# Optimization experiments

Measured on AMD Instinct MI355X. Metric: run time of the kernel, lower is better.

The kernel has to match this reference:

```python
import jax, jax.numpy as jnp
import numpy as np

B, C, H, W = 2, 32, 256, 1216
PT = 6
EPS = 1e-6

def _conv(x, w):
    # 3x3 conv, stride 1, SAME padding, NCHW/OIHW
    return jax.lax.conv_general_dilated(x, w, (1, 1), ((1, 1), (1, 1)),
                                        dimension_numbers=('NCHW', 'OIHW', 'NCHW'))

def _cbn(x, w, s, b):
    # conv (bias=False) + eval-mode BatchNorm folded into per-channel scale/bias
    return _conv(x, w) * s[None, :, None, None] + b[None, :, None, None]

def _cb(x, w, b):
    # conv with bias (no norm branch of Basic2d)
    return _conv(x, w) + b[None, :, None, None]

def _gen_kernel(fout, w1, s1, b1, w2, s2, b2):
    # GenKernel: normalized per-pixel kernel with middle weight = 1 - sum(others)
    h = jax.nn.relu(_cbn(fout, w1, s1, b1))
    w = _cbn(h, w2, s2, b2)  # [B, pk*pk-1, H, W]
    w = w / (jnp.sum(jnp.abs(w), axis=1, keepdims=True) + EPS)
    wmid = 1.0 - jnp.sum(w, axis=1, keepdims=True)
    half = w.shape[1] // 2
    return jnp.concatenate([w[:, :half], wmid, w[:, half:]], axis=1)  # [B, pk*pk, H, W]

def _local_conv(x, w, k):
    # bpconvlocal: per-pixel spatially-varying k x k convolution of a 1-channel map
    p = k // 2
    _, _, Hx, Wx = x.shape
    xp = jnp.pad(x, ((0, 0), (0, 0), (p, p), (p, p)))
    patches = jnp.stack([xp[:, 0, i:i + Hx, j:j + Wx]
                         for i in range(k) for j in range(k)], axis=1)  # [B, k*k, H, W]
    return jnp.sum(w * patches, axis=1, keepdims=True)

def _cspn(fout, hn, h0,
          k3w1, k3s1, k3b1, k3w2, k3s2, k3b2,
          k5w1, k5s1, k5b1, k5w2, k5s2, k5b2,
          k7w1, k7s1, k7b1, k7w2, k7s2, k7b2,
          mw1, ms1, mb1, mw2, mbias2,
          cw1, cs1, cb1, cw2, cbias2,
          tw1, ts1, tb1, tw2, tbias2):
    w3 = _gen_kernel(fout, k3w1, k3s1, k3b1, k3w2, k3s2, k3b2)
    w5 = _gen_kernel(fout, k5w1, k5s1, k5b1, k5w2, k5s2, k5b2)
    w7 = _gen_kernel(fout, k7w1, k7s1, k7b1, k7w2, k7s2, k7b2)
    valid = (h0 > 0.001).astype(fout.dtype)
    mask = jax.nn.sigmoid(_cb(jax.nn.relu(_cbn(fout, mw1, ms1, mb1)), mw2, mbias2)) * valid
    m3, m5, m7 = jnp.split(mask, 3, axis=1)
    conf = jax.nn.softmax(_cb(jax.nn.relu(_cbn(fout, cw1, cs1, cb1)), cw2, cbias2), axis=1)
    c3, c5, c7 = jnp.split(conf, 3, axis=1)
    h3 = h5 = h7 = hn
    hns = [hn]
    for i in range(PT):
        h3 = (1.0 - m3) * _local_conv(h3, w3, 3) + m3 * h0
        h5 = (1.0 - m5) * _local_conv(h5, w5, 5) + m5 * h0
        h7 = (1.0 - m7) * _local_conv(h7, w7, 7) + m7 * h0
        if i == PT // 2 - 1:
            hns.append(c3 * h3 + c5 * h5 + c7 * h7)
    hns.append(c3 * h3 + c5 * h5 + c7 * h7)
    hns = jnp.concatenate(hns, axis=1)  # [B, 3, H, W]
    wt = jax.nn.softmax(_cb(jax.nn.relu(_cbn(jnp.concatenate([fout, hns], axis=1),
                                             tw1, ts1, tb1)), tw2, tbias2), axis=1)
    return jnp.sum(wt * hns, axis=1, keepdims=True)

def setup_inputs():
    key = jax.random.key(0)
    ks = iter(jax.random.split(key, 80))
    def nrm(shape, s=0.05):
        return jax.random.normal(next(ks), shape, dtype=jnp.float32) * s
    d = {}
    d['fout'] = jax.random.normal(next(ks), (B, C, H, W), dtype=jnp.float32)
    d['hn'] = jax.random.uniform(next(ks), (B, 1, H, W), dtype=jnp.float32) * 10.0
    sparse = (jax.random.uniform(next(ks), (B, 1, H, W)) < 0.06).astype(jnp.float32)
    d['h0'] = sparse * jax.random.uniform(next(ks), (B, 1, H, W), dtype=jnp.float32) * 10.0
    for pk, pre in ((3, 'k3'), (5, 'k5'), (7, 'k7')):
        co = pk * pk - 1
        d[pre + 'w1'] = nrm((C, C, 3, 3)); d[pre + 's1'] = 1.0 + nrm((C,)); d[pre + 'b1'] = nrm((C,))
        d[pre + 'w2'] = nrm((co, C, 3, 3)); d[pre + 's2'] = 1.0 + nrm((co,)); d[pre + 'b2'] = nrm((co,))
    for pre, cin in (('m', C), ('c', C), ('t', C + 3)):
        d[pre + 'w1'] = nrm((C, cin, 3, 3)); d[pre + 's1'] = 1.0 + nrm((C,)); d[pre + 'b1'] = nrm((C,))
        d[pre + 'w2'] = nrm((3, C, 3, 3)); d[pre + 'bias2'] = nrm((3,))
    return d

def reference(fout, hn, h0,
              k3w1, k3s1, k3b1, k3w2, k3s2, k3b2,
              k5w1, k5s1, k5b1, k5w2, k5s2, k5b2,
              k7w1, k7s1, k7b1, k7w2, k7s2, k7b2,
              mw1, ms1, mb1, mw2, mbias2,
              cw1, cs1, cb1, cw2, cbias2,
              tw1, ts1, tb1, tw2, tbias2):
    return _cspn(fout, hn, h0,
                 k3w1, k3s1, k3b1, k3w2, k3s2, k3b2,
                 k5w1, k5s1, k5b1, k5w2, k5s2, k5b2,
                 k7w1, k7s1, k7b1, k7w2, k7s2, k7b2,
                 mw1, ms1, mb1, mw2, mbias2,
                 cw1, cs1, cb1, cw2, cbias2,
                 tw1, ts1, tb1, tw2, tbias2)
```

## Files before the change

### kernel.cpp

```cpp
#include <hip/hip_runtime.h>
#include <hip/hip_bf16.h>

constexpr int B_ = 2, H_ = 256, W_ = 1216;
constexpr int HW = H_ * W_;
constexpr int NP = B_ * HW;
constexpr int WP = W_ + 2;
constexpr int HP = H_ + 2;
constexpr int HWP = HP * WP;
constexpr float EPS_ = 1e-6f;

constexpr int PW1_K3 = 0;
constexpr int PW1_K5 = 18432;
constexpr int PW1_K7 = 36864;
constexpr int PW2_K3 = 55296;
constexpr int PW2_K5 = 64512;
constexpr int PW2_K7 = 82944;
constexpr int PP1_M  = 110592;
constexpr int PP1_C  = 119808;
constexpr int PP1_T  = 129024;
constexpr int PP1T2  = 138240;
constexpr int PG2_M  = 140544;
constexpr int PG2_C  = 145152;
constexpr int PG2_T  = 149760;
constexpr int PREP_N = 154368;

typedef __bf16 bfrag __attribute__((ext_vector_type(8)));
typedef float f4 __attribute__((ext_vector_type(4)));

union BU { uint4 u; bfrag f; };

__device__ __forceinline__ ushort f2b(float x) {
  uint u = __float_as_uint(x);
  u += 0x7fffu + ((u >> 16) & 1u);
  return (ushort)(u >> 16);
}
__device__ __forceinline__ float b2f(ushort u) {
  return __uint_as_float(((uint)u) << 16);
}

__global__ __launch_bounds__(256)
void prep_k(const float* __restrict__ k3w1, const float* __restrict__ k5w1,
            const float* __restrict__ k7w1, const float* __restrict__ k3w2,
            const float* __restrict__ k5w2, const float* __restrict__ k7w2,
            const float* __restrict__ mw1, const float* __restrict__ cw1,
            const float* __restrict__ tw1, const float* __restrict__ mw2,
            const float* __restrict__ cw2, const float* __restrict__ tw2,
            ushort* __restrict__ wp)
{
  int i = blockIdx.x * 256 + threadIdx.x;
  if (i >= PREP_N) return;
  ushort outv;
  if (i < PW2_K3) {
    int c = i / 18432, r = i % 18432;
    const float* src = (c == 0) ? k3w1 : (c == 1) ? k5w1 : k7w1;
    int ci = r & 31; int t1 = r >> 5;
    int co = t1 & 31; int t2 = t1 >> 5;
    int tap = t2 % 9, half = t2 / 9;
    float v = src[(co * 32 + ci) * 9 + tap];
    ushort hi = f2b(v);
    outv = half ? f2b(v - b2f(hi)) : hi;
  } else if (i < PP1_M) {
    int r = i - PW2_K3;
    const float* src; int NM16, CO;
    if (r < 9216)       { src = k3w2; NM16 = 16; CO = 8; }
    else if (r < 27648) { src = k5w2; NM16 = 32; CO = 24; r -= 9216; }
    else                { src = k7w2; NM16 = 48; CO = 48; r -= 27648; }
    int ci = r & 31; int t1 = r >> 5;
    int co = t1 % NM16; int t2 = t1 / NM16;
    int tap = t2 % 9, half = t2 / 9;
    if (co < CO) {
      float v = src[(co * 32 + ci) * 9 + tap];
      ushort hi = f2b(v);
      outv = half ? f2b(v - b2f(hi)) : hi;
    } else outv = 0;
  } else if (i < PP1T2) {
    int r = i - PP1_M;
    int c = r / 9216; r %= 9216;
    const float* src = (c == 0) ? mw1 : (c == 1) ? cw1 : tw1;
    int CIN = (c == 2) ? 35 : 32;
    int ci = r & 31; int t1 = r >> 5;
    int co = t1 & 31, tap = t1 >> 5;
    outv = f2b(src[(co * CIN + ci) * 9 + tap]);
  } else if (i < PG2_M) {
    int r = i - PP1T2;
    int c8 = r & 7; int t1 = r >> 3;
    int co = t1 & 31, tap = t1 >> 5;
    int cc = (c8 < 3) ? c8 : ((c8 < 6) ? c8 - 3 : -1);
    outv = (cc >= 0) ? f2b(tw1[(co * 35 + 32 + cc) * 9 + tap]) : (ushort)0;
  } else {
    int r = i - PG2_M;
    int c = r / 4608; r %= 4608;
    const float* src = (c == 0) ? mw2 : (c == 1) ? cw2 : tw2;
    int ci = r & 31; int t1 = r >> 5;
    int co = t1 & 15, tap = t1 >> 4;
    outv = (co < 3) ? f2b(src[(co * 32 + ci) * 9 + tap]) : (ushort)0;
  }
  wp[i] = outv;
}

__global__ __launch_bounds__(256)
void zring_k(ushort* __restrict__ hP) {
  constexpr int PB = 2 * WP * 4 + 2 * (HP - 2) * 4;
  int i = blockIdx.x * 256 + threadIdx.x;
  if (i >= 2 * PB) return;
  int b = i / PB, r = i % PB;
  size_t idx;
  if (r < WP * 4) idx = (size_t)r;
  else if (r < 2 * WP * 4) idx = (size_t)(HP - 1) * WP * 4 + (r - WP * 4);
  else {
    int q = r - 2 * WP * 4;
    int row = q >> 3, k = q & 7;
    int col = (k < 4) ? k : (WP - 1) * 4 + (k - 4);
    idx = (size_t)(row + 1) * WP * 4 + col;
  }
  *(uint4*)&hP[(size_t)b * HWP * 32 + idx * 8] = uint4{0, 0, 0, 0};
}

__global__ __launch_bounds__(256, 3)
void convs1(const float* __restrict__ xf, const ushort* __restrict__ wp,
            const float* __restrict__ scale, const float* __restrict__ bias,
            ushort* __restrict__ outh)
{
  __shared__ ushort xl[25344];

  const int tid = threadIdx.x;
  const int lane = tid & 63;
  const int wid = tid >> 6;
  const int x0 = blockIdx.x * 64, y0 = blockIdx.y * 4, b = blockIdx.z;

  for (int i = tid; i < 396 * 4; i += 256) {
    int oct = i & 3, rest = i >> 2;
    int xx = rest % 66, rr = rest / 66;
    int yy = y0 - 1 + rr, x = x0 - 1 + xx;
    uint4 vh = {0, 0, 0, 0}, vl = {0, 0, 0, 0};
    if ((unsigned)yy < (unsigned)H_ && (unsigned)x < (unsigned)W_) {
      const float* src = xf + ((size_t)b * 32 + oct * 8) * HW + (size_t)yy * W_ + x;
      uint uh[4], ul[4];
#pragma unroll
      for (int j = 0; j < 4; ++j) {
        float a = src[(size_t)(2 * j + 0) * HW];
        float c = src[(size_t)(2 * j + 1) * HW];
        ushort ah = f2b(a), ch = f2b(c);
        ushort al = f2b(a - b2f(ah)), cl = f2b(c - b2f(ch));
        uh[j] = (uint)ah | ((uint)ch << 16);
        ul[j] = (uint)al | ((uint)cl << 16);
      }
      vh = uint4{uh[0], uh[1], uh[2], uh[3]};
      vl = uint4{ul[0], ul[1], ul[2], ul[3]};
    }
    *(uint4*)&xl[rest * 32 + oct * 8] = vh;
    *(uint4*)&xl[12672 + rest * 32 + oct * 8] = vl;
  }
  __syncthreads();

  const int n = lane & 15, quad = lane >> 4;

  f4 acc[4][2];
#pragma unroll
  for (int tu = 0; tu < 4; ++tu)
#pragma unroll
    for (int mt = 0; mt < 2; ++mt) acc[tu][mt] = f4{0.f, 0.f, 0.f, 0.f};

#pragma unroll
  for (int tap = 0; tap < 9; ++tap) {
    int dy = tap / 3, dx = tap % 3;
    bfrag avhi[2], avlo[2];
#pragma unroll
    for (int mt = 0; mt < 2; ++mt) {
      avhi[mt] = *(const bfrag*)&wp[((tap * 32) + mt * 16 + n) * 32 + quad * 8];
      avlo[mt] = *(const bfrag*)&wp[(((9 + tap) * 32) + mt * 16 + n) * 32 + quad * 8];
    }
#pragma unroll
    for (int tu = 0; tu < 4; ++tu) {
      int t = wid + tu * 4;
      int r = t >> 2, g = t & 3;
      int pix = (r + dy) * 66 + g * 16 + n + dx;
      bfrag bhi = *(const bfrag*)&xl[pix * 32 + quad * 8];
      bfrag blo = *(const bfrag*)&xl[12672 + pix * 32 + quad * 8];
#pragma unroll
      for (int mt = 0; mt < 2; ++mt) {
        acc[tu][mt] = __builtin_amdgcn_mfma_f32_16x16x32_bf16(avhi[mt], bhi, acc[tu][mt], 0, 0, 0);
        acc[tu][mt] = __builtin_amdgcn_mfma_f32_16x16x32_bf16(avhi[mt], blo, acc[tu][mt], 0, 0, 0);
        acc[tu][mt] = __builtin_amdgcn_mfma_f32_16x16x32_bf16(avlo[mt], bhi, acc[tu][mt], 0, 0, 0);
      }
    }
  }

#pragma unroll
  for (int tu = 0; tu < 4; ++tu) {
    int t = wid + tu * 4;
    int r = t >> 2, g = t & 3;
    int gx = x0 + g * 16 + n, gy = y0 + r;
    size_t bpix = (size_t)b * HWP + (size_t)(gy + 1) * WP + (gx + 1);
#pragma unroll
    for (int mt = 0; mt < 2; ++mt) {
      int cob = mt * 16 + quad * 4;
      float v0 = fmaxf(acc[tu][mt][0] * scale[cob + 0] + bias[cob + 0], 0.f);
      float v1 = fmaxf(acc[tu][mt][1] * scale[cob + 1] + bias[cob + 1], 0.f);
      float v2 = fmaxf(acc[tu][mt][2] * scale[cob + 2] + bias[cob + 2], 0.f);
      float v3 = fmaxf(acc[tu][mt][3] * scale[cob + 3] + bias[cob + 3], 0.f);
      uint u0 = (uint)f2b(v0) | ((uint)f2b(v1) << 16);
      uint u1 = (uint)f2b(v2) | ((uint)f2b(v3) << 16);
      *(uint2*)&outh[bpix * 32 + cob] = uint2{u0, u1};
    }
  }
}

template<int nM, int MINW>
__global__ __launch_bounds__(256, MINW)
void convs2(const ushort* __restrict__ hP, const ushort* __restrict__ wp,
            const float* __restrict__ scale, const float* __restrict__ bias,
            ushort* __restrict__ outw, int CO)
{
  constexpr int NM16 = nM * 16;
  const int tid = threadIdx.x;
  const int lane = tid & 63;
  const int wid = tid >> 6;
  const int x0 = blockIdx.x * 64, y0 = blockIdx.y * 4, b = blockIdx.z;

  const int n = lane & 15, quad = lane >> 4;
  const ushort* hb = hP + (size_t)b * HWP * 32;

  f4 acc[4][nM];
#pragma unroll
  for (int tu = 0; tu < 4; ++tu)
#pragma unroll
    for (int mt = 0; mt < nM; ++mt) acc[tu][mt] = f4{0.f, 0.f, 0.f, 0.f};

#pragma unroll
  for (int tap = 0; tap < 9; ++tap) {
    int dy = tap / 3, dx = tap % 3;
    bfrag whi[nM], wlo[nM];
#pragma unroll
    for (int mt = 0; mt < nM; ++mt) {
      whi[mt] = *(const bfrag*)&wp[((tap * NM16) + mt * 16 + n) * 32 + quad * 8];
      wlo[mt] = *(const bfrag*)&wp[((9 * NM16) + tap * NM16 + mt * 16 + n) * 32 + quad * 8];
    }
#pragma unroll
    for (int tu = 0; tu < 4; ++tu) {
      int t = wid + tu * 4;
      int r = t >> 2, g = t & 3;
      int rb = (y0 + r + dy) * WP + x0 + g * 16 + n + dx;
      bfrag bv = *(const bfrag*)&hb[(size_t)rb * 32 + quad * 8];
#pragma unroll
      for (int mt = 0; mt < nM; ++mt) {
        acc[tu][mt] = __builtin_amdgcn_mfma_f32_16x16x32_bf16(whi[mt], bv, acc[tu][mt], 0, 0, 0);
        acc[tu][mt] = __builtin_amdgcn_mfma_f32_16x16x32_bf16(wlo[mt], bv, acc[tu][mt], 0, 0, 0);
      }
    }
  }

#pragma unroll
  for (int tu = 0; tu < 4; ++tu) {
    int t = wid + tu * 4;
    int r = t >> 2, g = t & 3;
    int gx = x0 + g * 16 + n, gy = y0 + r;
    size_t gpix = (size_t)gy * W_ + gx;

    float vs[nM][4];
    float pa = 0.f;
#pragma unroll
    for (int mt = 0; mt < nM; ++mt)
#pragma unroll
      for (int rg = 0; rg < 4; ++rg) {
        int co = mt * 16 + quad * 4 + rg;
        float v = (co < CO) ? acc[tu][mt][rg] * scale[co] + bias[co] : 0.f;
        vs[mt][rg] = v;
        pa += fabsf(v);
      }
    pa += __shfl_xor(pa, 16);
    pa += __shfl_xor(pa, 32);
    float inv = 1.f / (pa + EPS_);
#pragma unroll
    for (int mt = 0; mt < nM; ++mt)
#pragma unroll
      for (int rg = 0; rg < 4; ++rg) {
        int co = mt * 16 + quad * 4 + rg;
        if (co < CO)
          outw[((size_t)b * CO + co) * HW + gpix] = f2b(vs[mt][rg] * inv);
      }
  }
}

template<int KB2, int MINW>
__global__ __launch_bounds__(256, MINW)
void conv1p(const float* __restrict__ xf, const float* __restrict__ hnsp,
            const ushort* __restrict__ wp, const ushort* __restrict__ wp2,
            const float* __restrict__ scale, const float* __restrict__ bias,
            ushort* __restrict__ outh)
{
  __shared__ ushort xl[396 * 32];
  __shared__ ushort xl2[KB2 ? 396 * 8 : 8];

  const int tid = threadIdx.x;
  const int lane = tid & 63;
  const int wid = tid >> 6;
  const int x0 = blockIdx.x * 64, y0 = blockIdx.y * 4, b = blockIdx.z;

  if (KB2) {
    for (int i = tid; i < 396; i += 256) {
      int xx = i % 66, rr = i / 66;
      int yy = y0 - 1 + rr, x = x0 - 1 + xx;
      float v0 = 0.f, v1 = 0.f, v2 = 0.f;
      if ((unsigned)yy < (unsigned)H_ && (unsigned)x < (unsigned)W_) {
        size_t pix = (size_t)yy * W_ + x;
        v0 = hnsp[((size_t)b * 3 + 0) * HW + pix];
        v1 = hnsp[((size_t)b * 3 + 1) * HW + pix];
        v2 = hnsp[((size_t)b * 3 + 2) * HW + pix];
      }
      ushort h0b = f2b(v0), h1b = f2b(v1), h2b = f2b(v2);
      ushort l0 = f2b(v0 - b2f(h0b)), l1 = f2b(v1 - b2f(h1b)), l2 = f2b(v2 - b2f(h2b));
      uint u0 = (uint)h0b | ((uint)h1b << 16);
      uint u1 = (uint)h2b | ((uint)l0 << 16);
      uint u2 = (uint)l1 | ((uint)l2 << 16);
      *(uint4*)&xl2[i * 8] = uint4{u0, u1, u2, 0};
    }
  }
  for (int i = tid; i < 396 * 4; i += 256) {
    int oct = i & 3, rest = i >> 2;
    int xx = rest % 66, rr = rest / 66;
    int yy = y0 - 1 + rr, x = x0 - 1 + xx;
    uint4 v = {0, 0, 0, 0};
    if ((unsigned)yy < (unsigned)H_ && (unsigned)x < (unsigned)W_) {
      const float* src = xf + ((size_t)b * 32 + oct * 8) * HW + (size_t)yy * W_ + x;
      uint u[4];
#pragma unroll
      for (int j = 0; j < 4; ++j) {
        float a = src[(size_t)(2 * j + 0) * HW];
        float c = src[(size_t)(2 * j + 1) * HW];
        u[j] = (uint)f2b(a) | ((uint)f2b(c) << 16);
      }
      v = uint4{u[0], u[1], u[2], u[3]};
    }
    *(uint4*)&xl[rest * 32 + oct * 8] = v;
  }
  __syncthreads();

  const int n = lane & 15, quad = lane >> 4;

  f4 acc[4][2];
#pragma unroll
  for (int tu = 0; tu < 4; ++tu)
#pragma unroll
    for (int mt = 0; mt < 2; ++mt) acc[tu][mt] = f4{0.f, 0.f, 0.f, 0.f};

#pragma unroll
  for (int tap = 0; tap < 9; ++tap) {
    int dy = tap / 3, dx = tap % 3;
    bfrag av[2];
#pragma unroll
    for (int mt = 0; mt < 2; ++mt)
      av[mt] = *(const bfrag*)&wp[((tap * 32) + mt * 16 + n) * 32 + quad * 8];
    bfrag a2[KB2 ? 2 : 1];
    if (KB2) {
#pragma unroll
      for (int mt = 0; mt < 2; ++mt) {
        BU t; t.u = uint4{0, 0, 0, 0};
        if (lane < 16) t.f = *(const bfrag*)&wp2[(tap * 32 + mt * 16 + lane) * 8];
        a2[mt] = t.f;
      }
    }
#pragma unroll
    for (int tu = 0; tu < 4; ++tu) {
      int t = wid + tu * 4;
      int r = t >> 2, g = t & 3;
      int pix = (r + dy) * 66 + g * 16 + n + dx;
      bfrag bv = *(const bfrag*)&xl[pix * 32 + quad * 8];
#pragma unroll
      for (int mt = 0; mt < 2; ++mt)
        acc[tu][mt] = __builtin_amdgcn_mfma_f32_16x16x32_bf16(av[mt], bv, acc[tu][mt], 0, 0, 0);
      if (KB2) {
        BU t2; t2.u = uint4{0, 0, 0, 0};
        if (lane < 16) t2.f = *(const bfrag*)&xl2[pix * 8];
#pragma unroll
        for (int mt = 0; mt < 2; ++mt)
          acc[tu][mt] = __builtin_amdgcn_mfma_f32_16x16x32_bf16(a2[mt], t2.f, acc[tu][mt], 0, 0, 0);
      }
    }
  }

#pragma unroll
  for (int tu = 0; tu < 4; ++tu) {
    int t = wid + tu * 4;
    int r = t >> 2, g = t & 3;
    int gx = x0 + g * 16 + n, gy = y0 + r;
    size_t bpix = (size_t)b * HWP + (size_t)(gy + 1) * WP + (gx + 1);
#pragma unroll
    for (int mt = 0; mt < 2; ++mt) {
      int cob = mt * 16 + quad * 4;
      float v0 = fmaxf(acc[tu][mt][0] * scale[cob + 0] + bias[cob + 0], 0.f);
      float v1 = fmaxf(acc[tu][mt][1] * scale[cob + 1] + bias[cob + 1], 0.f);
      float v2 = fmaxf(acc[tu][mt][2] * scale[cob + 2] + bias[cob + 2], 0.f);
      float v3 = fmaxf(acc[tu][mt][3] * scale[cob + 3] + bias[cob + 3], 0.f);
      uint u0 = (uint)f2b(v0) | ((uint)f2b(v1) << 16);
      uint u1 = (uint)f2b(v2) | ((uint)f2b(v3) << 16);
      *(uint2*)&outh[bpix * 32 + cob] = uint2{u0, u1};
    }
  }
}

template<int EPI>
__global__ __launch_bounds__(256, 4)
void conv2g(const ushort* __restrict__ hP, const ushort* __restrict__ wp,
            const float* __restrict__ bias, const float* __restrict__ h0,
            const float* __restrict__ hnsp, float* __restrict__ outf)
{
  const int tid = threadIdx.x;
  const int lane = tid & 63;
  const int wid = tid >> 6;
  const int x0 = blockIdx.x * 64, y0 = blockIdx.y * 4, b = blockIdx.z;
  const int n = lane & 15, quad = lane >> 4;

  bfrag av[9];
#pragma unroll
  for (int tap = 0; tap < 9; ++tap)
    av[tap] = *(const bfrag*)&wp[((tap * 16) + n) * 32 + quad * 8];

  const ushort* hb = hP + (size_t)b * HWP * 32;

  f4 acc[4];
#pragma unroll
  for (int tu = 0; tu < 4; ++tu) acc[tu] = f4{0.f, 0.f, 0.f, 0.f};

#pragma unroll
  for (int tap = 0; tap < 9; ++tap) {
    int dy = tap / 3, dx = tap % 3;
#pragma unroll
    for (int tu = 0; tu < 4; ++tu) {
      int t = wid + tu * 4;
      int r = t >> 2, g = t & 3;
      int rb = (y0 + r + dy) * WP + x0 + g * 16 + n + dx;
      bfrag bv = *(const bfrag*)&hb[(size_t)rb * 32 + quad * 8];
      acc[tu] = __builtin_amdgcn_mfma_f32_16x16x32_bf16(av[tap], bv, acc[tu], 0, 0, 0);
    }
  }

#pragma unroll
  for (int tu = 0; tu < 4; ++tu) {
    int t = wid + tu * 4;
    int r = t >> 2, g = t & 3;
    int gx = x0 + g * 16 + n, gy = y0 + r;
    size_t gpix = (size_t)gy * W_ + gx;
    size_t bpix = (size_t)b * HW + gpix;

    if constexpr (EPI == 2) {
      if (lane < 16) {
        float valid = (h0[bpix] > 0.001f) ? 1.f : 0.f;
#pragma unroll
        for (int rg = 0; rg < 3; ++rg) {
          float v = acc[tu][rg] + bias[rg];
          float sg = 1.f / (1.f + expf(-v));
          outf[((size_t)b * 3 + rg) * HW + gpix] = sg * valid;
        }
      }
    } else if constexpr (EPI == 3) {
      if (lane < 16) {
        float v0 = acc[tu][0] + bias[0];
        float v1 = acc[tu][1] + bias[1];
        float v2 = acc[tu][2] + bias[2];
        float m = fmaxf(v0, fmaxf(v1, v2));
        float e0 = expf(v0 - m), e1 = expf(v1 - m), e2 = expf(v2 - m);
        float inv = 1.f / (e0 + e1 + e2);
        outf[((size_t)b * 3 + 0) * HW + gpix] = e0 * inv;
        outf[((size_t)b * 3 + 1) * HW + gpix] = e1 * inv;
        outf[((size_t)b * 3 + 2) * HW + gpix] = e2 * inv;
      }
    } else if constexpr (EPI == 4) {
      if (lane < 16) {
        float v0 = acc[tu][0] + bias[0];
        float v1 = acc[tu][1] + bias[1];
        float v2 = acc[tu][2] + bias[2];
        float m = fmaxf(v0, fmaxf(v1, v2));
        float e0 = expf(v0 - m), e1 = expf(v1 - m), e2 = expf(v2 - m);
        float inv = 1.f / (e0 + e1 + e2);
        float a0 = hnsp[((size_t)b * 3 + 0) * HW + gpix];
        float a1 = hnsp[((size_t)b * 3 + 1) * HW + gpix];
        float a2v = hnsp[((size_t)b * 3 + 2) * HW + gpix];
        outf[bpix] = (e0 * a0 + e1 * a1 + e2 * a2v) * inv;
      }
    }
  }
}

__global__ __launch_bounds__(256)
void init_k(const float* __restrict__ hn, float* __restrict__ h3,
            float* __restrict__ h5, float* __restrict__ h7,
            float* __restrict__ hns)
{
  int t = blockIdx.x * 256 + threadIdx.x;
  if (t >= NP) return;
  float v = hn[t];
  h3[t] = v; h5[t] = v; h7[t] = v;
  int b = t / HW, rem = t - b * HW;
  hns[(size_t)b * 3 * HW + rem] = v;
}

__global__ __launch_bounds__(256)
void iterate_k(const float* __restrict__ h3i, const float* __restrict__ h5i,
               const float* __restrict__ h7i,
               float* __restrict__ h3o, float* __restrict__ h5o,
               float* __restrict__ h7o,
               const ushort* __restrict__ w3, const ushort* __restrict__ w5,
               const ushort* __restrict__ w7,
               const float* __restrict__ mask, const float* __restrict__ h0,
               float* __restrict__ hns, int chn, const float* __restrict__ conf)
{
  int t = blockIdx.x * 256 + threadIdx.x;
  if (t >= NP) return;
  int b = t / HW;
  int rem = t - b * HW;
  int y = rem / W_;
  int x = rem - y * W_;
  size_t pb = (size_t)b * HW;

  float h0v = h0[t];

  float s3 = 0.f, ws3 = 0.f;
#pragma unroll
  for (int p = 0; p < 8; ++p) {
    int tap = (p < 4) ? p : p + 1;
    int dy = tap / 3 - 1, dx = tap % 3 - 1;
    int yy = y + dy, xx = x + dx;
    float hv = ((unsigned)yy < (unsigned)H_ && (unsigned)xx < (unsigned)W_)
                   ? h3i[pb + yy * W_ + xx] : 0.f;
    float wv = b2f(w3[(size_t)(b * 8 + p) * HW + rem]);
    ws3 += wv;
    s3 += wv * hv;
  }
  s3 += (1.f - ws3) * h3i[t];
  float m3 = mask[(size_t)(b * 3 + 0) * HW + rem];
  float n3 = (1.f - m3) * s3 + m3 * h0v;
  h3o[t] = n3;

  float s5 = 0.f, ws5 = 0.f;
#pragma unroll
  for (int p = 0; p < 24; ++p) {
    int tap = (p < 12) ? p : p + 1;
    int dy = tap / 5 - 2, dx = tap % 5 - 2;
    int yy = y + dy, xx = x + dx;
    float hv = ((unsigned)yy < (unsigned)H_ && (unsigned)xx < (unsigned)W_)
                   ? h5i[pb + yy * W_ + xx] : 0.f;
    float wv = b2f(w5[(size_t)(b * 24 + p) * HW + rem]);
    ws5 += wv;
    s5 += wv * hv;
  }
  s5 += (1.f - ws5) * h5i[t];
  float m5 = mask[(size_t)(b * 3 + 1) * HW + rem];
  float n5 = (1.f - m5) * s5 + m5 * h0v;
  h5o[t] = n5;

  float s7 = 0.f, ws7 = 0.f;
#pragma unroll
  for (int p = 0; p < 48; ++p) {
    int tap = (p < 24) ? p : p + 1;
    int dy = tap / 7 - 3, dx = tap % 7 - 3;
    int yy = y + dy, xx = x + dx;
    float hv = ((unsigned)yy < (unsigned)H_ && (unsigned)xx < (unsigned)W_)
                   ? h7i[pb + yy * W_ + xx] : 0.f;
    float wv = b2f(w7[(size_t)(b * 48 + p) * HW + rem]);
    ws7 += wv;
    s7 += wv * hv;
  }
  s7 += (1.f - ws7) * h7i[t];
  float m7 = mask[(size_t)(b * 3 + 2) * HW + rem];
  float n7 = (1.f - m7) * s7 + m7 * h0v;
  h7o[t] = n7;

  if (chn >= 0) {
    float c3 = conf[(size_t)(b * 3 + 0) * HW + rem];
    float c5 = conf[(size_t)(b * 3 + 1) * HW + rem];
    float c7 = conf[(size_t)(b * 3 + 2) * HW + rem];
    hns[(size_t)(b * 3 + chn) * HW + rem] = c3 * n3 + c5 * n5 + c7 * n7;
  }
}

extern "C" void kernel_launch(void* const* d_in, const int* in_sizes, int n_in,
                              void* d_out, int out_size, void* d_ws, size_t ws_size,
                              hipStream_t stream) {
  const float* fout = (const float*)d_in[0];
  const float* hn   = (const float*)d_in[1];
  const float* h0   = (const float*)d_in[2];
  const float* k3w1 = (const float*)d_in[3];
  const float* k3s1 = (const float*)d_in[4];
  const float* k3b1 = (const float*)d_in[5];
  const float* k3w2 = (const float*)d_in[6];
  const float* k3s2 = (const float*)d_in[7];
  const float* k3b2 = (const float*)d_in[8];
  const float* k5w1 = (const float*)d_in[9];
  const float* k5s1 = (const float*)d_in[10];
  const float* k5b1 = (const float*)d_in[11];
  const float* k5w2 = (const float*)d_in[12];
  const float* k5s2 = (const float*)d_in[13];
  const float* k5b2 = (const float*)d_in[14];
  const float* k7w1 = (const float*)d_in[15];
  const float* k7s1 = (const float*)d_in[16];
  const float* k7b1 = (const float*)d_in[17];
  const float* k7w2 = (const float*)d_in[18];
  const float* k7s2 = (const float*)d_in[19];
  const float* k7b2 = (const float*)d_in[20];
  const float* mw1  = (const float*)d_in[21];
  const float* ms1  = (const float*)d_in[22];
  const float* mb1  = (const float*)d_in[23];
  const float* mw2  = (const float*)d_in[24];
  const float* mbias2 = (const float*)d_in[25];
  const float* cw1  = (const float*)d_in[26];
  const float* cs1  = (const float*)d_in[27];
  const float* cb1  = (const float*)d_in[28];
  const float* cw2  = (const float*)d_in[29];
  const float* cbias2 = (const float*)d_in[30];
  const float* tw1  = (const float*)d_in[31];
  const float* ts1  = (const float*)d_in[32];
  const float* tb1  = (const float*)d_in[33];
  const float* tw2  = (const float*)d_in[34];
  const float* tbias2 = (const float*)d_in[35];

  float* out = (float*)d_out;

  size_t hP_elems = (size_t)2 * HWP * 32;
  size_t need = hP_elems * 2 + (size_t)NP * (80 * 2 + 15 * 4) + (size_t)PREP_N * 2;
  if (ws_size < need) return;
  ushort* hPb  = (ushort*)d_ws;
  ushort* w3   = hPb  + hP_elems;
  ushort* w5   = w3   + (size_t)8 * NP;
  ushort* w7   = w5   + (size_t)24 * NP;
  float* mask  = (float*)(w7 + (size_t)48 * NP);
  float* conf  = mask + (size_t)3 * NP;
  float* hA    = conf + (size_t)3 * NP;
  float* hns   = hA   + (size_t)6 * NP;
  ushort* wp   = (ushort*)(hns + (size_t)3 * NP);

  dim3 blk(256);
  dim3 gc(W_ / 64, H_ / 4, B_);
  int ge = NP / 256;
  constexpr int PB = 2 * WP * 4 + 2 * (HP - 2) * 4;
  int gz = (2 * PB + 255) / 256;
  int gp = (PREP_N + 255) / 256;

  prep_k<<<gp, blk, 0, stream>>>(k3w1, k5w1, k7w1, k3w2, k5w2, k7w2,
                                 mw1, cw1, tw1, mw2, cw2, tw2, wp);
  zring_k<<<gz, blk, 0, stream>>>(hPb);

  convs1<<<gc, blk, 0, stream>>>(fout, wp + PW1_K3, k3s1, k3b1, hPb);
  convs2<1, 4><<<gc, blk, 0, stream>>>(hPb, wp + PW2_K3, k3s2, k3b2, w3, 8);
  convs1<<<gc, blk, 0, stream>>>(fout, wp + PW1_K5, k5s1, k5b1, hPb);
  convs2<2, 4><<<gc, blk, 0, stream>>>(hPb, wp + PW2_K5, k5s2, k5b2, w5, 24);
  convs1<<<gc, blk, 0, stream>>>(fout, wp + PW1_K7, k7s1, k7b1, hPb);
  convs2<3, 3><<<gc, blk, 0, stream>>>(hPb, wp + PW2_K7, k7s2, k7b2, w7, 48);

  conv1p<0, 4><<<gc, blk, 0, stream>>>(fout, nullptr, wp + PP1_M, nullptr, ms1, mb1, hPb);
  conv2g<2><<<gc, blk, 0, stream>>>(hPb, wp + PG2_M, mbias2, h0, nullptr, mask);

  conv1p<0, 4><<<gc, blk, 0, stream>>>(fout, nullptr, wp + PP1_C, nullptr, cs1, cb1, hPb);
  conv2g<3><<<gc, blk, 0, stream>>>(hPb, wp + PG2_C, cbias2, nullptr, nullptr, conf);

  float* h3c = hA + (size_t)0 * NP; float* h3n = hA + (size_t)1 * NP;
  float* h5c = hA + (size_t)2 * NP; float* h5n = hA + (size_t)3 * NP;
  float* h7c = hA + (size_t)4 * NP; float* h7n = hA + (size_t)5 * NP;

  init_k<<<ge, blk, 0, stream>>>(hn, h3c, h5c, h7c, hns);
  for (int i = 0; i < 6; ++i) {
    int chn = (i == 2) ? 1 : ((i == 5) ? 2 : -1);
    iterate_k<<<ge, blk, 0, stream>>>(h3c, h5c, h7c, h3n, h5n, h7n,
                                      w3, w5, w7, mask, h0, hns, chn, conf);
    float* t;
    t = h3c; h3c = h3n; h3n = t;
    t = h5c; h5c = h5n; h5n = t;
    t = h7c; h7c = h7n; h7n = t;
  }

  conv1p<1, 3><<<gc, blk, 0, stream>>>(fout, hns, wp + PP1_T, wp + PP1T2, ts1, tb1, hPb);
  conv2g<4><<<gc, blk, 0, stream>>>(hPb, wp + PG2_T, tbias2, nullptr, hns, out);
}
```

Before: 916.7 us.

## Stage conv inputs in LDS, double-buffer weights, store kernel weights pixel-major

Both the second-stage kernel-generation conv and the 1-output conv now stage the 6x66 padded input tile into shared memory and read it from there, instead of issuing repeated global loads for each of the nine taps. Per-tap weight fragments are prefetched one tap ahead with a double buffer. The generated per-pixel weights are now written pixel-major (channels contiguous), so the propagation kernel can fetch them with 16-byte vector loads instead of strided scalar loads. The propagation kernel reads these weights six times per call. The trade-off is more shared memory per block, which may lower occupancy, and lane-strided 8-byte stores in the conv epilogue.

```diff
diff --git a/kernel.cpp b/kernel.cpp
--- a/kernel.cpp
+++ b/kernel.cpp
@@ -28,6 +28,7 @@
 typedef float f4 __attribute__((ext_vector_type(4)));
 
 union BU { uint4 u; bfrag f; };
+union U8 { uint4 u; ushort s[8]; };
 
 __device__ __forceinline__ ushort f2b(float x) {
   uint u = __float_as_uint(x);
@@ -212,14 +213,23 @@
             const float* __restrict__ scale, const float* __restrict__ bias,
             ushort* __restrict__ outw, int CO)
 {
+  __shared__ ushort xl[12672];
+
   constexpr int NM16 = nM * 16;
   const int tid = threadIdx.x;
   const int lane = tid & 63;
   const int wid = tid >> 6;
   const int x0 = blockIdx.x * 64, y0 = blockIdx.y * 4, b = blockIdx.z;
+  const ushort* hb = hP + (size_t)b * HWP * 32;
+
+  for (int i = tid; i < 396 * 4; i += 256) {
+    int oct = i & 3, rest = i >> 2;
+    int xx = rest % 66, rr = rest / 66;
+    *(uint4*)&xl[rest * 32 + oct * 8] =
+        *(const uint4*)&hb[((size_t)(y0 + rr) * WP + (x0 + xx)) * 32 + oct * 8];
+  }
 
   const int n = lane & 15, quad = lane >> 4;
-  const ushort* hb = hP + (size_t)b * HWP * 32;
 
   f4 acc[4][nM];
 #pragma unroll
@@ -227,25 +237,35 @@
 #pragma unroll
     for (int mt = 0; mt < nM; ++mt) acc[tu][mt] = f4{0.f, 0.f, 0.f, 0.f};
 
+  bfrag whi[2][nM], wlo[2][nM];
+#pragma unroll
+  for (int mt = 0; mt < nM; ++mt) {
+    whi[0][mt] = *(const bfrag*)&wp[(mt * 16 + n) * 32 + quad * 8];
+    wlo[0][mt] = *(const bfrag*)&wp[((9 * NM16) + mt * 16 + n) * 32 + quad * 8];
+  }
+  __syncthreads();
+
 #pragma unroll
   for (int tap = 0; tap < 9; ++tap) {
-    int dy = tap / 3, dx = tap % 3;
-    bfrag whi[nM], wlo[nM];
-#pragma unroll
-    for (int mt = 0; mt < nM; ++mt) {
-      whi[mt] = *(const bfrag*)&wp[((tap * NM16) + mt * 16 + n) * 32 + quad * 8];
-      wlo[mt] = *(const bfrag*)&wp[((9 * NM16) + tap * NM16 + mt * 16 + n) * 32 + quad * 8];
+    const int dy = tap / 3, dx = tap % 3;
+    const int cur = tap & 1, nxt = cur ^ 1;
+    if (tap < 8) {
+#pragma unroll
+      for (int mt = 0; mt < nM; ++mt) {
+        whi[nxt][mt] = *(const bfrag*)&wp[(((tap + 1) * NM16) + mt * 16 + n) * 32 + quad * 8];
+        wlo[nxt][mt] = *(const bfrag*)&wp[(((9 + tap + 1) * NM16) + mt * 16 + n) * 32 + quad * 8];
+      }
     }
 #pragma unroll
     for (int tu = 0; tu < 4; ++tu) {
       int t = wid + tu * 4;
       int r = t >> 2, g = t & 3;
-      int rb = (y0 + r + dy) * WP + x0 + g * 16 + n + dx;
-      bfrag bv = *(const bfrag*)&hb[(size_t)rb * 32 + quad * 8];
+      int pix = (r + dy) * 66 + g * 16 + n + dx;
+      bfrag bv = *(const bfrag*)&xl[pix * 32 + quad * 8];
 #pragma unroll
       for (int mt = 0; mt < nM; ++mt) {
-        acc[tu][mt] = __builtin_amdgcn_mfma_f32_16x16x32_bf16(whi[mt], bv, acc[tu][mt], 0, 0, 0);
-        acc[tu][mt] = __builtin_amdgcn_mfma_f32_16x16x32_bf16(wlo[mt], bv, acc[tu][mt], 0, 0, 0);
+        acc[tu][mt] = __builtin_amdgcn_mfma_f32_16x16x32_bf16(whi[cur][mt], bv, acc[tu][mt], 0, 0, 0);
+        acc[tu][mt] = __builtin_amdgcn_mfma_f32_16x16x32_bf16(wlo[cur][mt], bv, acc[tu][mt], 0, 0, 0);
       }
     }
   }
@@ -271,14 +291,17 @@
     pa += __shfl_xor(pa, 16);
     pa += __shfl_xor(pa, 32);
     float inv = 1.f / (pa + EPS_);
-#pragma unroll
-    for (int mt = 0; mt < nM; ++mt)
-#pragma unroll
-      for (int rg = 0; rg < 4; ++rg) {
-        int co = mt * 16 + quad * 4 + rg;
-        if (co < CO)
-          outw[((size_t)b * CO + co) * HW + gpix] = f2b(vs[mt][rg] * inv);
-      }
+
+    size_t base = ((size_t)b * HW + gpix) * (size_t)CO;
+#pragma unroll
+    for (int mt = 0; mt < nM; ++mt) {
+      int cob = mt * 16 + quad * 4;
+      if (cob < CO) {
+        uint u0 = (uint)f2b(vs[mt][0] * inv) | ((uint)f2b(vs[mt][1] * inv) << 16);
+        uint u1 = (uint)f2b(vs[mt][2] * inv) | ((uint)f2b(vs[mt][3] * inv) << 16);
+        *(uint2*)&outw[base + cob] = uint2{u0, u1};
+      }
+    }
   }
 }
 
@@ -405,22 +428,31 @@
             const float* __restrict__ bias, const float* __restrict__ h0,
             const float* __restrict__ hnsp, float* __restrict__ outf)
 {
+  __shared__ ushort xl[12672];
+
   const int tid = threadIdx.x;
   const int lane = tid & 63;
   const int wid = tid >> 6;
   const int x0 = blockIdx.x * 64, y0 = blockIdx.y * 4, b = blockIdx.z;
   const int n = lane & 15, quad = lane >> 4;
+  const ushort* hb = hP + (size_t)b * HWP * 32;
+
+  for (int i = tid; i < 396 * 4; i += 256) {
+    int oct = i & 3, rest = i >> 2;
+    int xx = rest % 66, rr = rest / 66;
+    *(uint4*)&xl[rest * 32 + oct * 8] =
+        *(const uint4*)&hb[((size_t)(y0 + rr) * WP + (x0 + xx)) * 32 + oct * 8];
+  }
 
   bfrag av[9];
 #pragma unroll
   for (int tap = 0; tap < 9; ++tap)
     av[tap] = *(const bfrag*)&wp[((tap * 16) + n) * 32 + quad * 8];
 
-  const ushort* hb = hP + (size_t)b * HWP * 32;
-
   f4 acc[4];
 #pragma unroll
   for (int tu = 0; tu < 4; ++tu) acc[tu] = f4{0.f, 0.f, 0.f, 0.f};
+  __syncthreads();
 
 #pragma unroll
   for (int tap = 0; tap < 9; ++tap) {
@@ -429,8 +461,8 @@
     for (int tu = 0; tu < 4; ++tu) {
       int t = wid + tu * 4;
       int r = t >> 2, g = t & 3;
-      int rb = (y0 + r + dy) * WP + x0 + g * 16 + n + dx;
-      bfrag bv = *(const bfrag*)&hb[(size_t)rb * 32 + quad * 8];
+      int pix = (r + dy) * 66 + g * 16 + n + dx;
+      bfrag bv = *(const bfrag*)&xl[pix * 32 + quad * 8];
       acc[tu] = __builtin_amdgcn_mfma_f32_16x16x32_bf16(av[tap], bv, acc[tu], 0, 0, 0);
     }
   }
@@ -515,6 +547,7 @@
 
   float h0v = h0[t];
 
+  U8 a3; a3.u = *(const uint4*)&w3[((size_t)b * HW + rem) * 8];
   float s3 = 0.f, ws3 = 0.f;
 #pragma unroll
   for (int p = 0; p < 8; ++p) {
@@ -523,7 +556,7 @@
     int yy = y + dy, xx = x + dx;
     float hv = ((unsigned)yy < (unsigned)H_ && (unsigned)xx < (unsigned)W_)
                    ? h3i[pb + yy * W_ + xx] : 0.f;
-    float wv = b2f(w3[(size_t)(b * 8 + p) * HW + rem]);
+    float wv = b2f(a3.s[p]);
     ws3 += wv;
     s3 += wv * hv;
   }
@@ -532,6 +565,12 @@
   float n3 = (1.f - m3) * s3 + m3 * h0v;
   h3o[t] = n3;
 
+  U8 a5[3];
+  {
+    const ushort* w5r = w5 + ((size_t)b * HW + rem) * 24;
+#pragma unroll
+    for (int q = 0; q < 3; ++q) a5[q].u = *(const uint4*)(w5r + q * 8);
+  }
   float s5 = 0.f, ws5 = 0.f;
 #pragma unroll
   for (int p = 0; p < 24; ++p) {
@@ -540,7 +579,7 @@
     int yy = y + dy, xx = x + dx;
     float hv = ((unsigned)yy < (unsigned)H_ && (unsigned)xx < (unsigned)W_)
                    ? h5i[pb + yy * W_ + xx] : 0.f;
-    float wv = b2f(w5[(size_t)(b * 24 + p) * HW + rem]);
+    float wv = b2f(a5[p >> 3].s[p & 7]);
     ws5 += wv;
     s5 += wv * hv;
   }
@@ -549,6 +588,12 @@
   float n5 = (1.f - m5) * s5 + m5 * h0v;
   h5o[t] = n5;
 
+  U8 a7[6];
+  {
+    const ushort* w7r = w7 + ((size_t)b * HW + rem) * 48;
+#pragma unroll
+    for (int q = 0; q < 6; ++q) a7[q].u = *(const uint4*)(w7r + q * 8);
+  }
   float s7 = 0.f, ws7 = 0.f;
 #pragma unroll
   for (int p = 0; p < 48; ++p) {
@@ -557,7 +602,7 @@
     int yy = y + dy, xx = x + dx;
     float hv = ((unsigned)yy < (unsigned)H_ && (unsigned)xx < (unsigned)W_)
                    ? h7i[pb + yy * W_ + xx] : 0.f;
-    float wv = b2f(w7[(size_t)(b * 48 + p) * HW + rem]);
+    float wv = b2f(a7[p >> 3].s[p & 7]);
     ws7 += wv;
     s7 += wv * hv;
   }
```

Result: no change. 899.2 us, median of 2 (-1.9%).
